# Optimization experiments

Hardware: AMD Instinct MI355X
Metric: run time of the kernel (lower is better)

The kernel has to match this reference:

```python
import jax, jax.numpy as jnp
import numpy as np

EMBED_DIM = 768
NUM_HEADS = 12
HEAD_DIM = EMBED_DIM // NUM_HEADS
SCALING = HEAD_DIM ** -0.5
B, S = 2, 2048


def setup_inputs() -> dict:
    key = jax.random.key(0)
    k1, k2, k3 = jax.random.split(key, 3)
    x_q = jax.random.normal(k1, (B, S, EMBED_DIM), dtype=jnp.float32)
    # xavier-uniform-ish scaling for weights
    lim_qkv = (6.0 / (EMBED_DIM + 3 * EMBED_DIM)) ** 0.5
    lim_out = (6.0 / (2 * EMBED_DIM)) ** 0.5
    w_qkv = jax.random.uniform(k2, (3 * EMBED_DIM, EMBED_DIM), jnp.float32, -lim_qkv, lim_qkv)
    b_qkv = jnp.zeros((3 * EMBED_DIM,), jnp.float32)
    w_out = jax.random.uniform(k3, (EMBED_DIM, EMBED_DIM), jnp.float32, -lim_out, lim_out)
    b_out = jnp.zeros((EMBED_DIM,), jnp.float32)
    return {"x_q": x_q, "w_qkv": w_qkv, "b_qkv": b_qkv, "w_out": w_out, "b_out": b_out}


def reference(x_q, w_qkv, b_qkv, w_out, b_out):
    b_sz, s_len, _ = x_q.shape
    # qkv projection: (B,S,3E) -> (B,S,3,H,hd) -> split
    qkv = x_q @ w_qkv.T + b_qkv
    qkv = qkv.reshape(b_sz, s_len, 3, NUM_HEADS, HEAD_DIM)
    q = qkv[:, :, 0].transpose(0, 2, 1, 3) * SCALING  # (B,H,S,hd)
    k = qkv[:, :, 1].transpose(0, 2, 1, 3)
    v = qkv[:, :, 2].transpose(0, 2, 1, 3)
    attn = jnp.einsum("bhsd,bhtd->bhst", q, k)  # (B,H,S,S)
    attn = jax.nn.softmax(attn.astype(jnp.float32), axis=-1).astype(attn.dtype)
    out = jnp.einsum("bhst,bhtd->bhsd", attn, v)  # (B,H,S,hd)
    out = out.transpose(0, 2, 1, 3).reshape(b_sz, s_len, EMBED_DIM)
    return out @ w_out.T + b_out
```

## Files before the change

kernel.cpp:

```cpp
#include <hip/hip_runtime.h>
#include <hip/hip_bf16.h>
#include <math.h>

typedef unsigned short u16;
typedef unsigned int u32;
typedef __attribute__((ext_vector_type(8))) short bf16x8;
typedef __attribute__((ext_vector_type(4))) short bf16x4;
typedef __attribute__((ext_vector_type(4))) float f32x4;

#define EMBED 768
#define NHEADS 12
#define HDIM 64
#define NBATCH 2
#define SEQ 2048
#define NTOK 4096
#define QKV_N 2304
#define BHTOT 24
#define QSCALE 0.18033688011112042f

__device__ __forceinline__ u16 f2b(float f) {
    __hip_bfloat16 h = __float2bfloat16(f);
    return __builtin_bit_cast(u16, h);
}
__device__ __forceinline__ u32 pk2(float a, float b) {
    return (u32)f2b(a) | ((u32)f2b(b) << 16);
}
__device__ __forceinline__ f32x4 mfma32(bf16x8 a, bf16x8 b, f32x4 c) {
    return __builtin_amdgcn_mfma_f32_16x16x32_bf16(a, b, c, 0, 0, 0);
}
#if __has_builtin(__builtin_amdgcn_mfma_f32_16x16x16_bf16)
__device__ __forceinline__ f32x4 mfma16(bf16x4 a, bf16x4 b, f32x4 c) {
    return __builtin_amdgcn_mfma_f32_16x16x16_bf16(a, b, c, 0, 0, 0);
}
#else
__device__ __forceinline__ f32x4 mfma16(bf16x4 a, bf16x4 b, f32x4 c) {
    return __builtin_amdgcn_mfma_f32_16x16x16bf16_1k(a, b, c, 0, 0, 0);
}
#endif

__device__ __forceinline__ float exp2_hw(float x) {
#if __has_builtin(__builtin_amdgcn_exp2f)
    return __builtin_amdgcn_exp2f(x);
#else
    float r;
    asm("v_exp_f32 %0, %1" : "=v"(r) : "v"(x));
    return r;
#endif
}

__device__ __forceinline__ void async16(const u16* g, u16* l) {
    __builtin_amdgcn_global_load_lds(
        (const __attribute__((address_space(1))) unsigned int*)g,
        (__attribute__((address_space(3))) unsigned int*)l,
        16, 0, 0);
}

__global__ __launch_bounds__(256)
void cast_kernel(const float* __restrict__ s0, u16* __restrict__ d0, int n0,
                 const float* __restrict__ s1, u16* __restrict__ d1, int n1,
                 const float* __restrict__ s2, u16* __restrict__ d2, int n2)
{
    int idx = (blockIdx.x * 256 + threadIdx.x) * 4;
    const float* s; u16* d; int i;
    if (idx < n0)            { s = s0; d = d0; i = idx; }
    else if (idx < n0 + n1)  { s = s1; d = d1; i = idx - n0; }
    else                     { s = s2; d = d2; i = idx - n0 - n1; if (i >= n2) return; }
    float4 v = *(const float4*)&s[i];
    ushort4 o;
    o.x = f2b(v.x); o.y = f2b(v.y); o.z = f2b(v.z); o.w = f2b(v.w);
    *(ushort4*)&d[i] = o;
}

__global__ __launch_bounds__(256)
void qkv_gemm(const u16* __restrict__ A, const u16* __restrict__ W,
              const float* __restrict__ bias,
              u16* __restrict__ Qb, u16* __restrict__ Kb, u16* __restrict__ VT)
{
    __shared__ __align__(16) u16 smem[4 * 8192];
    u16* As = smem;
    u16* Bs = smem + 2 * 8192;
    const int m0 = blockIdx.x * 128;
    const int n0 = blockIdx.y * 128;
    const int tid = threadIdx.x;
    const int w = tid >> 6, l = tid & 63;
    const int c = l & 15, q = l >> 4;
    const int wm = (w >> 1) * 64, wn = (w & 1) * 64;
    const int r8 = l >> 3, ch = l & 7;
    const int gch = ch ^ r8;

    #pragma unroll
    for (int j = 0; j < 4; ++j) {
        int row = w * 32 + j * 8 + r8;
        int seg = (w * 32 + j * 8) * 64;
        async16(&A[(size_t)(m0 + row) * EMBED + gch * 8], &As[seg + l * 8]);
        async16(&W[(size_t)(n0 + row) * EMBED + gch * 8], &Bs[seg + l * 8]);
    }

    f32x4 acc[4][4] = {};
    const int NK = EMBED / 64;

    #pragma unroll 2
    for (int kt = 0; kt < NK; ++kt) {
        const int cur = kt & 1;
        __syncthreads();
        if (kt + 1 < NK) {
            int k0 = (kt + 1) * 64;
            #pragma unroll
            for (int j = 0; j < 4; ++j) {
                int row = w * 32 + j * 8 + r8;
                int seg = (cur ^ 1) * 8192 + (w * 32 + j * 8) * 64;
                async16(&A[(size_t)(m0 + row) * EMBED + k0 + gch * 8], &As[seg + l * 8]);
                async16(&W[(size_t)(n0 + row) * EMBED + k0 + gch * 8], &Bs[seg + l * 8]);
            }
        }
        const u16* Ab = As + cur * 8192;
        const u16* Bb = Bs + cur * 8192;
        #pragma unroll
        for (int ks = 0; ks < 2; ++ks) {
            const int cs = (((ks << 2) | q) ^ (c & 7)) << 3;
            bf16x8 af[4], bfr[4];
            #pragma unroll
            for (int i = 0; i < 4; ++i)
                af[i] = *(const bf16x8*)&Ab[(wm + i * 16 + c) * 64 + cs];
            #pragma unroll
            for (int j = 0; j < 4; ++j)
                bfr[j] = *(const bf16x8*)&Bb[(wn + j * 16 + c) * 64 + cs];
            #pragma unroll
            for (int i = 0; i < 4; ++i)
                #pragma unroll
                for (int j = 0; j < 4; ++j)
                    acc[i][j] = mfma32(af[i], bfr[j], acc[i][j]);
        }
    }

    const int p = n0 / EMBED;
    const int ncol0 = n0 + wn;
    const int h = (ncol0 % EMBED) / HDIM;
    const int mrow0 = m0 + wm;
    const int b = mrow0 >> 11;
    const int s0 = mrow0 & (SEQ - 1);

    if (p < 2) {
        u16* dst = (p == 0) ? Qb : Kb;
        const float mul = (p == 0) ? QSCALE : 1.0f;
        #pragma unroll
        for (int j = 0; j < 4; ++j) {
            int n = ncol0 + j * 16 + c;
            int d = j * 16 + c;
            float bval = bias[n];
            #pragma unroll
            for (int i = 0; i < 4; ++i) {
                #pragma unroll
                for (int r = 0; r < 4; ++r) {
                    int s = s0 + i * 16 + q * 4 + r;
                    float v = (acc[i][j][r] + bval) * mul;
                    dst[(((size_t)(b * NHEADS + h)) * SEQ + s) * HDIM + d] = f2b(v);
                }
            }
        }
    } else {
        __syncthreads();
        u16* T = smem + w * (64 * 72);
        #pragma unroll
        for (int j = 0; j < 4; ++j) {
            int n = ncol0 + j * 16 + c;
            float bval = bias[n];
            #pragma unroll
            for (int i = 0; i < 4; ++i) {
                uint2 pr;
                pr.x = pk2(acc[i][j][0] + bval, acc[i][j][1] + bval);
                pr.y = pk2(acc[i][j][2] + bval, acc[i][j][3] + bval);
                *(uint2*)&T[(j * 16 + c) * 72 + i * 16 + q * 4] = pr;
            }
        }
        const size_t vtbase = ((size_t)(b * NHEADS + h)) * HDIM * SEQ + s0;
        #pragma unroll
        for (int ii = 0; ii < 8; ++ii) {
            int d = (l >> 3) + 8 * ii;
            int sch = (l & 7) * 8;
            uint4 vv = *(const uint4*)&T[d * 72 + sch];
            *(uint4*)&VT[vtbase + (size_t)d * SEQ + sch] = vv;
        }
    }
}

__global__ __launch_bounds__(256, 3)
void attn_kernel(const u16* __restrict__ Qb, const u16* __restrict__ Kb,
                 const u16* __restrict__ VT, u16* __restrict__ AO)
{
    __shared__ __align__(16) u16 Ks[3][4096];
    __shared__ __align__(16) u16 Vs[3][4096];

    const int blk = blockIdx.x;
    const int g = blk & 7, kk = blk >> 3;
    const int bh = g * 3 + (kk >> 5);
    const int qt = kk & 31;

    const int tid = threadIdx.x;
    const int w = tid >> 6, l = tid & 63;
    const int c = l & 15, q = l >> 4;

    const u16* qg = Qb + ((size_t)bh * SEQ + qt * 64 + w * 16) * HDIM;
    const u16* kg = Kb + ((size_t)bh * SEQ) * HDIM;
    const u16* vg = VT + ((size_t)bh * HDIM) * SEQ;

    const int r8 = l >> 3, ch = l & 7;
    const int gch = ch ^ r8;

    bf16x8 bq0 = *(const bf16x8*)&qg[c * HDIM + q * 8];
    bf16x8 bq1 = *(const bf16x8*)&qg[c * HDIM + 32 + q * 8];

    f32x4 o[4] = {};
    float lrow = 0.f;

    const int NT = SEQ / 64;

#define STAGE(JT, BS) {                                                       \
    int row0 = w * 16 + r8;                                                   \
    async16(&kg[(size_t)((JT) * 64 + row0) * HDIM + gch * 8],                 \
            &Ks[BS][(w * 16) * 64 + l * 8]);                                  \
    async16(&vg[(size_t)row0 * SEQ + (JT) * 64 + gch * 8],                    \
            &Vs[BS][(w * 16) * 64 + l * 8]);                                  \
    async16(&kg[(size_t)((JT) * 64 + row0 + 8) * HDIM + gch * 8],             \
            &Ks[BS][(w * 16 + 8) * 64 + l * 8]);                              \
    async16(&vg[(size_t)(row0 + 8) * SEQ + (JT) * 64 + gch * 8],              \
            &Vs[BS][(w * 16 + 8) * 64 + l * 8]);                              \
}

#define QKT(SN, BN) {                                                         \
    __builtin_amdgcn_s_setprio(1);                                            \
    _Pragma("unroll")                                                         \
    for (int kb = 0; kb < 4; ++kb) {                                          \
        bf16x8 ak0 = *(const bf16x8*)&Ks[BN][(kb * 16 + c) * 64 +             \
                                             (((q    ) ^ (c & 7)) << 3)];     \
        bf16x8 ak1 = *(const bf16x8*)&Ks[BN][(kb * 16 + c) * 64 +             \
                                             (((q | 4) ^ (c & 7)) << 3)];     \
        f32x4 zz = {};                                                        \
        zz = mfma32(ak0, bq0, zz);                                            \
        SN[kb] = mfma32(ak1, bq1, zz);                                        \
    }                                                                         \
    __builtin_amdgcn_s_setprio(0);                                            \
}

#define SOFTPV(SC, BC) {                                                      \
    _Pragma("unroll")                                                         \
    for (int kb = 0; kb < 4; ++kb) {                                          \
        float p0 = exp2_hw(SC[kb][0]);                                        \
        float p1 = exp2_hw(SC[kb][1]);                                        \
        float p2 = exp2_hw(SC[kb][2]);                                        \
        float p3 = exp2_hw(SC[kb][3]);                                        \
        SC[kb][0] = p0; SC[kb][1] = p1; SC[kb][2] = p2; SC[kb][3] = p3;       \
        lrow += (p0 + p1) + (p2 + p3);                                        \
    }                                                                         \
    bf16x4 bp[4];                                                             \
    _Pragma("unroll")                                                         \
    for (int kb = 0; kb < 4; ++kb) {                                          \
        uint2 pr;                                                             \
        pr.x = pk2(SC[kb][0], SC[kb][1]);                                     \
        pr.y = pk2(SC[kb][2], SC[kb][3]);                                     \
        bp[kb] = __builtin_bit_cast(bf16x4, pr);                              \
    }                                                                         \
    __builtin_amdgcn_s_setprio(1);                                            \
    _Pragma("unroll")                                                         \
    for (int db = 0; db < 4; ++db) {                                          \
        bf16x4 av[4];                                                         \
        _Pragma("unroll")                                                     \
        for (int kb = 0; kb < 4; ++kb)                                        \
            av[kb] = *(const bf16x4*)&Vs[BC][(db * 16 + c) * 64 +             \
                      (((2 * kb + (q >> 1)) ^ (c & 7)) << 3) + ((q & 1) << 2)]; \
        f32x4 t = o[db];                                                      \
        _Pragma("unroll")                                                     \
        for (int kb = 0; kb < 4; ++kb) t = mfma16(av[kb], bp[kb], t);         \
        o[db] = t;                                                            \
    }                                                                         \
    __builtin_amdgcn_s_setprio(0);                                            \
}

#define BODY(J, SC, SN, BC, BN, BS) {                                         \
    asm volatile("s_waitcnt vmcnt(0)" ::: "memory");                          \
    __builtin_amdgcn_s_barrier();                                             \
    if ((J) + 2 < NT) STAGE((J) + 2, BS);                                     \
    if ((J) + 1 < NT) QKT(SN, BN);                                            \
    SOFTPV(SC, BC);                                                           \
}

    f32x4 scA[4], scB[4];

    STAGE(0, 0);
    STAGE(1, 1);
    asm volatile("s_waitcnt vmcnt(4)" ::: "memory");
    __builtin_amdgcn_s_barrier();
    QKT(scA, 0);

    for (int jb = 0; jb < 30; jb += 6) {
        BODY(jb + 0, scA, scB, 0, 1, 2);
        BODY(jb + 1, scB, scA, 1, 2, 0);
        BODY(jb + 2, scA, scB, 2, 0, 1);
        BODY(jb + 3, scB, scA, 0, 1, 2);
        BODY(jb + 4, scA, scB, 1, 2, 0);
        BODY(jb + 5, scB, scA, 2, 0, 1);
    }
    BODY(30, scA, scB, 0, 1, 2);
    SOFTPV(scB, 1);

#undef STAGE
#undef QKT
#undef SOFTPV
#undef BODY

    lrow += __shfl_xor(lrow, 16);
    lrow += __shfl_xor(lrow, 32);
    float inv = 1.0f / lrow;

    const int b = bh / NHEADS, h = bh % NHEADS;
    const int s = qt * 64 + w * 16 + c;
    u16* ao = AO + ((size_t)(b * SEQ + s)) * EMBED + h * HDIM;
    #pragma unroll
    for (int db = 0; db < 4; ++db) {
        uint2 oo;
        oo.x = pk2(o[db][0] * inv, o[db][1] * inv);
        oo.y = pk2(o[db][2] * inv, o[db][3] * inv);
        *(uint2*)&ao[db * 16 + q * 4] = oo;
    }
}

__global__ __launch_bounds__(256)
void out_gemm(const u16* __restrict__ A, const u16* __restrict__ W,
              const float* __restrict__ bias, float* __restrict__ out)
{
    __shared__ __align__(16) u16 As[2][8192];
    __shared__ __align__(16) u16 Bs[2][4096];
    const int m0 = blockIdx.x * 128;
    const int n0 = blockIdx.y * 64;
    const int tid = threadIdx.x;
    const int w = tid >> 6, l = tid & 63;
    const int c = l & 15, q = l >> 4;
    const int wm = w * 32;
    const int r8 = l >> 3, ch = l & 7;
    const int gch = ch ^ r8;

    #pragma unroll
    for (int j = 0; j < 4; ++j) {
        int row = w * 32 + j * 8 + r8;
        async16(&A[(size_t)(m0 + row) * EMBED + gch * 8],
                &As[0][(w * 32 + j * 8) * 64 + l * 8]);
    }
    #pragma unroll
    for (int j = 0; j < 2; ++j) {
        int row = w * 16 + j * 8 + r8;
        async16(&W[(size_t)(n0 + row) * EMBED + gch * 8],
                &Bs[0][(w * 16 + j * 8) * 64 + l * 8]);
    }

    f32x4 acc[2][4] = {};
    const int NK = EMBED / 64;

    #pragma unroll 2
    for (int kt = 0; kt < NK; ++kt) {
        const int cur = kt & 1;
        __syncthreads();
        if (kt + 1 < NK) {
            int k0 = (kt + 1) * 64;
            #pragma unroll
            for (int j = 0; j < 4; ++j) {
                int row = w * 32 + j * 8 + r8;
                async16(&A[(size_t)(m0 + row) * EMBED + k0 + gch * 8],
                        &As[cur ^ 1][(w * 32 + j * 8) * 64 + l * 8]);
            }
            #pragma unroll
            for (int j = 0; j < 2; ++j) {
                int row = w * 16 + j * 8 + r8;
                async16(&W[(size_t)(n0 + row) * EMBED + k0 + gch * 8],
                        &Bs[cur ^ 1][(w * 16 + j * 8) * 64 + l * 8]);
            }
        }
        #pragma unroll
        for (int ks = 0; ks < 2; ++ks) {
            const int cs = (((ks << 2) | q) ^ (c & 7)) << 3;
            bf16x8 af[2], bfr[4];
            #pragma unroll
            for (int i = 0; i < 2; ++i)
                af[i] = *(const bf16x8*)&As[cur][(wm + i * 16 + c) * 64 + cs];
            #pragma unroll
            for (int j = 0; j < 4; ++j)
                bfr[j] = *(const bf16x8*)&Bs[cur][(j * 16 + c) * 64 + cs];
            #pragma unroll
            for (int i = 0; i < 2; ++i)
                #pragma unroll
                for (int j = 0; j < 4; ++j)
                    acc[i][j] = mfma32(af[i], bfr[j], acc[i][j]);
        }
    }

    #pragma unroll
    for (int j = 0; j < 4; ++j) {
        int n = n0 + j * 16 + c;
        float bval = bias[n];
        #pragma unroll
        for (int i = 0; i < 2; ++i) {
            #pragma unroll
            for (int r = 0; r < 4; ++r) {
                int m = m0 + wm + i * 16 + q * 4 + r;
                out[(size_t)m * EMBED + n] = acc[i][j][r] + bval;
            }
        }
    }
}

extern "C" void kernel_launch(void* const* d_in, const int* in_sizes, int n_in,
                              void* d_out, int out_size, void* d_ws, size_t ws_size,
                              hipStream_t stream)
{
    const float* x    = (const float*)d_in[0];
    const float* wqkv = (const float*)d_in[1];
    const float* bqkv = (const float*)d_in[2];
    const float* wout = (const float*)d_in[3];
    const float* bout = (const float*)d_in[4];
    float* out = (float*)d_out;

    const int nx  = NTOK * EMBED;
    const int nwq = QKV_N * EMBED;
    const int nwo = EMBED * EMBED;
    const size_t per = (size_t)NBATCH * NHEADS * SEQ * HDIM;

    u16* xb    = (u16*)d_ws;
    u16* wqkvb = xb + nx;
    u16* woutb = wqkvb + nwq;
    u16* Qb    = woutb + nwo;
    u16* Kb    = Qb + per;
    u16* VT    = Kb + per;
    u16* AO    = VT + per;

    int castTot = (nx + nwq + nwo) / 4;
    cast_kernel<<<castTot / 256, 256, 0, stream>>>(x, xb, nx, wqkv, wqkvb, nwq, wout, woutb, nwo);

    dim3 g1(NTOK / 128, QKV_N / 128);
    qkv_gemm<<<g1, 256, 0, stream>>>(xb, wqkvb, bqkv, Qb, Kb, VT);

    attn_kernel<<<BHTOT * 32, 256, 0, stream>>>(Qb, Kb, VT, AO);

    dim3 g3(NTOK / 128, EMBED / 64);
    out_gemm<<<g3, 256, 0, stream>>>(AO, woutb, bout, out);
}
```

Baseline: 155.2 us.

## Split attention KV tile across waves instead of query rows, reduce via LDS

Each wave now handles all 64 query rows of the block against its own 16-key slice of each KV tile, instead of 16 query rows against all 64 keys. K and V fragment loads from LDS drop to one per wave per step, while Q fragments held in registers grow fourfold and the accumulators grow to 4x4 tiles. A cross-wave reduction of the partial outputs and row sums through LDS scratch, with several barriers, is added at the end. The intent is to cut LDS read traffic in the inner loop, at the cost of more register pressure under the launch bound of 3 blocks and a longer epilogue.

```diff
diff --git a/kernel.cpp b/kernel.cpp
--- a/kernel.cpp
+++ b/kernel.cpp
@@ -200,18 +200,22 @@
     const int w = tid >> 6, l = tid & 63;
     const int c = l & 15, q = l >> 4;
 
-    const u16* qg = Qb + ((size_t)bh * SEQ + qt * 64 + w * 16) * HDIM;
+    const u16* qg = Qb + ((size_t)bh * SEQ + qt * 64) * HDIM;
     const u16* kg = Kb + ((size_t)bh * SEQ) * HDIM;
     const u16* vg = VT + ((size_t)bh * HDIM) * SEQ;
 
     const int r8 = l >> 3, ch = l & 7;
     const int gch = ch ^ r8;
 
-    bf16x8 bq0 = *(const bf16x8*)&qg[c * HDIM + q * 8];
-    bf16x8 bq1 = *(const bf16x8*)&qg[c * HDIM + 32 + q * 8];
-
-    f32x4 o[4] = {};
-    float lrow = 0.f;
+    bf16x8 bq[4][2];
+    #pragma unroll
+    for (int qb = 0; qb < 4; ++qb) {
+        bq[qb][0] = *(const bf16x8*)&qg[(qb * 16 + c) * HDIM + q * 8];
+        bq[qb][1] = *(const bf16x8*)&qg[(qb * 16 + c) * HDIM + 32 + q * 8];
+    }
+
+    f32x4 o[4][4] = {};
+    float lrow[4] = {0.f, 0.f, 0.f, 0.f};
 
     const int NT = SEQ / 64;
 
@@ -229,49 +233,45 @@
 
 #define QKT(SN, BN) {                                                         \
     __builtin_amdgcn_s_setprio(1);                                            \
+    bf16x8 ak0 = *(const bf16x8*)&Ks[BN][(w * 16 + c) * 64 +                  \
+                                         (((q    ) ^ (c & 7)) << 3)];         \
+    bf16x8 ak1 = *(const bf16x8*)&Ks[BN][(w * 16 + c) * 64 +                  \
+                                         (((q | 4) ^ (c & 7)) << 3)];         \
     _Pragma("unroll")                                                         \
-    for (int kb = 0; kb < 4; ++kb) {                                          \
-        bf16x8 ak0 = *(const bf16x8*)&Ks[BN][(kb * 16 + c) * 64 +             \
-                                             (((q    ) ^ (c & 7)) << 3)];     \
-        bf16x8 ak1 = *(const bf16x8*)&Ks[BN][(kb * 16 + c) * 64 +             \
-                                             (((q | 4) ^ (c & 7)) << 3)];     \
+    for (int qb = 0; qb < 4; ++qb) {                                          \
         f32x4 zz = {};                                                        \
-        zz = mfma32(ak0, bq0, zz);                                            \
-        SN[kb] = mfma32(ak1, bq1, zz);                                        \
+        zz = mfma32(ak0, bq[qb][0], zz);                                      \
+        SN[qb] = mfma32(ak1, bq[qb][1], zz);                                  \
     }                                                                         \
     __builtin_amdgcn_s_setprio(0);                                            \
 }
 
 #define SOFTPV(SC, BC) {                                                      \
     _Pragma("unroll")                                                         \
-    for (int kb = 0; kb < 4; ++kb) {                                          \
-        float p0 = exp2_hw(SC[kb][0]);                                        \
-        float p1 = exp2_hw(SC[kb][1]);                                        \
-        float p2 = exp2_hw(SC[kb][2]);                                        \
-        float p3 = exp2_hw(SC[kb][3]);                                        \
-        SC[kb][0] = p0; SC[kb][1] = p1; SC[kb][2] = p2; SC[kb][3] = p3;       \
-        lrow += (p0 + p1) + (p2 + p3);                                        \
+    for (int qb = 0; qb < 4; ++qb) {                                          \
+        float p0 = exp2_hw(SC[qb][0]);                                        \
+        float p1 = exp2_hw(SC[qb][1]);                                        \
+        float p2 = exp2_hw(SC[qb][2]);                                        \
+        float p3 = exp2_hw(SC[qb][3]);                                        \
+        SC[qb][0] = p0; SC[qb][1] = p1; SC[qb][2] = p2; SC[qb][3] = p3;       \
+        lrow[qb] += (p0 + p1) + (p2 + p3);                                    \
     }                                                                         \
     bf16x4 bp[4];                                                             \
     _Pragma("unroll")                                                         \
-    for (int kb = 0; kb < 4; ++kb) {                                          \
+    for (int qb = 0; qb < 4; ++qb) {                                          \
         uint2 pr;                                                             \
-        pr.x = pk2(SC[kb][0], SC[kb][1]);                                     \
-        pr.y = pk2(SC[kb][2], SC[kb][3]);                                     \
-        bp[kb] = __builtin_bit_cast(bf16x4, pr);                              \
+        pr.x = pk2(SC[qb][0], SC[qb][1]);                                     \
+        pr.y = pk2(SC[qb][2], SC[qb][3]);                                     \
+        bp[qb] = __builtin_bit_cast(bf16x4, pr);                              \
     }                                                                         \
     __builtin_amdgcn_s_setprio(1);                                            \
     _Pragma("unroll")                                                         \
     for (int db = 0; db < 4; ++db) {                                          \
-        bf16x4 av[4];                                                         \
+        bf16x4 av = *(const bf16x4*)&Vs[BC][(db * 16 + c) * 64 +              \
+                  (((2 * w + (q >> 1)) ^ (c & 7)) << 3) + ((q & 1) << 2)];    \
         _Pragma("unroll")                                                     \
-        for (int kb = 0; kb < 4; ++kb)                                        \
-            av[kb] = *(const bf16x4*)&Vs[BC][(db * 16 + c) * 64 +             \
-                      (((2 * kb + (q >> 1)) ^ (c & 7)) << 3) + ((q & 1) << 2)]; \
-        f32x4 t = o[db];                                                      \
-        _Pragma("unroll")                                                     \
-        for (int kb = 0; kb < 4; ++kb) t = mfma16(av[kb], bp[kb], t);         \
-        o[db] = t;                                                            \
+        for (int qb = 0; qb < 4; ++qb)                                        \
+            o[db][qb] = mfma16(av, bp[qb], o[db][qb]);                        \
     }                                                                         \
     __builtin_amdgcn_s_setprio(0);                                            \
 }
@@ -308,9 +308,38 @@
 #undef SOFTPV
 #undef BODY
 
-    lrow += __shfl_xor(lrow, 16);
-    lrow += __shfl_xor(lrow, 32);
-    float inv = 1.0f / lrow;
+    __syncthreads();
+    float* SCR = (float*)&Ks[0][0];
+    float* LR  = (float*)&Vs[0][0];
+
+    #pragma unroll
+    for (int qb = 0; qb < 4; ++qb) {
+        lrow[qb] += __shfl_xor(lrow[qb], 16);
+        lrow[qb] += __shfl_xor(lrow[qb], 32);
+    }
+    if (q == 0) {
+        #pragma unroll
+        for (int qb = 0; qb < 4; ++qb)
+            LR[(w * 4 + qb) * 16 + c] = lrow[qb];
+    }
+
+    #pragma unroll
+    for (int db = 0; db < 4; ++db) {
+        __syncthreads();
+        #pragma unroll
+        for (int qb = 0; qb < 4; ++qb)
+            *(f32x4*)&SCR[(w * 4 + qb) * 320 + c * 20 + q * 4] = o[db][qb];
+        __syncthreads();
+        f32x4 s0 = *(const f32x4*)&SCR[(0 * 4 + w) * 320 + c * 20 + q * 4];
+        f32x4 s1 = *(const f32x4*)&SCR[(1 * 4 + w) * 320 + c * 20 + q * 4];
+        f32x4 s2 = *(const f32x4*)&SCR[(2 * 4 + w) * 320 + c * 20 + q * 4];
+        f32x4 s3 = *(const f32x4*)&SCR[(3 * 4 + w) * 320 + c * 20 + q * 4];
+        o[db][0] = (s0 + s1) + (s2 + s3);
+    }
+
+    float lsum = (LR[(0 * 4 + w) * 16 + c] + LR[(1 * 4 + w) * 16 + c]) +
+                 (LR[(2 * 4 + w) * 16 + c] + LR[(3 * 4 + w) * 16 + c]);
+    float inv = 1.0f / lsum;
 
     const int b = bh / NHEADS, h = bh % NHEADS;
     const int s = qt * 64 + w * 16 + c;
@@ -318,8 +347,8 @@
     #pragma unroll
     for (int db = 0; db < 4; ++db) {
         uint2 oo;
-        oo.x = pk2(o[db][0] * inv, o[db][1] * inv);
-        oo.y = pk2(o[db][2] * inv, o[db][3] * inv);
+        oo.x = pk2(o[db][0][0] * inv, o[db][0][1] * inv);
+        oo.y = pk2(o[db][0][2] * inv, o[db][0][3] * inv);
         *(uint2*)&ao[db * 16 + q * 4] = oo;
     }
 }
```

New measurement: 312.9 us. 2.02x slower.

## Split attention warps 2x2 over query and key halves with LDS reduction

Applied to the files above, without the earlier changes.

Each wave now handles 32 query rows against half of each 64-key tile, instead of 16 query rows against the full tile. Each K and V fragment read from LDS therefore feeds two query blocks, roughly halving per-wave LDS read traffic per MFMA. The two key-half partial outputs and row sums are combined through shared memory (reusing the K buffer) before normalization and store. In exchange, each wave holds more accumulator registers and the epilogue gains an extra LDS round trip with two barriers.

```diff
diff --git a/kernel.cpp b/kernel.cpp
--- a/kernel.cpp
+++ b/kernel.cpp
@@ -199,19 +199,24 @@
     const int tid = threadIdx.x;
     const int w = tid >> 6, l = tid & 63;
     const int c = l & 15, q = l >> 4;
-
-    const u16* qg = Qb + ((size_t)bh * SEQ + qt * 64 + w * 16) * HDIM;
+    const int wq = w >> 1, wk = w & 1;
+
+    const u16* qg = Qb + ((size_t)bh * SEQ + qt * 64 + wq * 32) * HDIM;
     const u16* kg = Kb + ((size_t)bh * SEQ) * HDIM;
     const u16* vg = VT + ((size_t)bh * HDIM) * SEQ;
 
     const int r8 = l >> 3, ch = l & 7;
     const int gch = ch ^ r8;
 
-    bf16x8 bq0 = *(const bf16x8*)&qg[c * HDIM + q * 8];
-    bf16x8 bq1 = *(const bf16x8*)&qg[c * HDIM + 32 + q * 8];
-
-    f32x4 o[4] = {};
-    float lrow = 0.f;
+    bf16x8 bq[2][2];
+    #pragma unroll
+    for (int qb2 = 0; qb2 < 2; ++qb2) {
+        bq[qb2][0] = *(const bf16x8*)&qg[(qb2 * 16 + c) * HDIM + q * 8];
+        bq[qb2][1] = *(const bf16x8*)&qg[(qb2 * 16 + c) * HDIM + 32 + q * 8];
+    }
+
+    f32x4 o[4][2] = {};
+    float lrow[2] = {0.f, 0.f};
 
     const int NT = SEQ / 64;
 
@@ -230,48 +235,56 @@
 #define QKT(SN, BN) {                                                         \
     __builtin_amdgcn_s_setprio(1);                                            \
     _Pragma("unroll")                                                         \
-    for (int kb = 0; kb < 4; ++kb) {                                          \
-        bf16x8 ak0 = *(const bf16x8*)&Ks[BN][(kb * 16 + c) * 64 +             \
+    for (int kb2 = 0; kb2 < 2; ++kb2) {                                       \
+        bf16x8 ak0 = *(const bf16x8*)&Ks[BN][(wk * 32 + kb2 * 16 + c) * 64 +  \
                                              (((q    ) ^ (c & 7)) << 3)];     \
-        bf16x8 ak1 = *(const bf16x8*)&Ks[BN][(kb * 16 + c) * 64 +             \
+        bf16x8 ak1 = *(const bf16x8*)&Ks[BN][(wk * 32 + kb2 * 16 + c) * 64 +  \
                                              (((q | 4) ^ (c & 7)) << 3)];     \
-        f32x4 zz = {};                                                        \
-        zz = mfma32(ak0, bq0, zz);                                            \
-        SN[kb] = mfma32(ak1, bq1, zz);                                        \
+        _Pragma("unroll")                                                     \
+        for (int qb2 = 0; qb2 < 2; ++qb2) {                                   \
+            f32x4 zz = {};                                                    \
+            zz = mfma32(ak0, bq[qb2][0], zz);                                 \
+            SN[kb2][qb2] = mfma32(ak1, bq[qb2][1], zz);                       \
+        }                                                                     \
     }                                                                         \
     __builtin_amdgcn_s_setprio(0);                                            \
 }
 
 #define SOFTPV(SC, BC) {                                                      \
     _Pragma("unroll")                                                         \
-    for (int kb = 0; kb < 4; ++kb) {                                          \
-        float p0 = exp2_hw(SC[kb][0]);                                        \
-        float p1 = exp2_hw(SC[kb][1]);                                        \
-        float p2 = exp2_hw(SC[kb][2]);                                        \
-        float p3 = exp2_hw(SC[kb][3]);                                        \
-        SC[kb][0] = p0; SC[kb][1] = p1; SC[kb][2] = p2; SC[kb][3] = p3;       \
-        lrow += (p0 + p1) + (p2 + p3);                                        \
-    }                                                                         \
-    bf16x4 bp[4];                                                             \
+    for (int kb2 = 0; kb2 < 2; ++kb2)                                         \
+        _Pragma("unroll")                                                     \
+        for (int qb2 = 0; qb2 < 2; ++qb2) {                                   \
+            float p0 = exp2_hw(SC[kb2][qb2][0]);                              \
+            float p1 = exp2_hw(SC[kb2][qb2][1]);                              \
+            float p2 = exp2_hw(SC[kb2][qb2][2]);                              \
+            float p3 = exp2_hw(SC[kb2][qb2][3]);                              \
+            SC[kb2][qb2][0] = p0; SC[kb2][qb2][1] = p1;                       \
+            SC[kb2][qb2][2] = p2; SC[kb2][qb2][3] = p3;                       \
+            lrow[qb2] += (p0 + p1) + (p2 + p3);                               \
+        }                                                                     \
+    bf16x4 bp[2][2];                                                          \
     _Pragma("unroll")                                                         \
-    for (int kb = 0; kb < 4; ++kb) {                                          \
-        uint2 pr;                                                             \
-        pr.x = pk2(SC[kb][0], SC[kb][1]);                                     \
-        pr.y = pk2(SC[kb][2], SC[kb][3]);                                     \
-        bp[kb] = __builtin_bit_cast(bf16x4, pr);                              \
-    }                                                                         \
+    for (int kb2 = 0; kb2 < 2; ++kb2)                                         \
+        _Pragma("unroll")                                                     \
+        for (int qb2 = 0; qb2 < 2; ++qb2) {                                   \
+            uint2 pr;                                                         \
+            pr.x = pk2(SC[kb2][qb2][0], SC[kb2][qb2][1]);                     \
+            pr.y = pk2(SC[kb2][qb2][2], SC[kb2][qb2][3]);                     \
+            bp[kb2][qb2] = __builtin_bit_cast(bf16x4, pr);                    \
+        }                                                                     \
     __builtin_amdgcn_s_setprio(1);                                            \
     _Pragma("unroll")                                                         \
     for (int db = 0; db < 4; ++db) {                                          \
-        bf16x4 av[4];                                                         \
+        bf16x4 av0 = *(const bf16x4*)&Vs[BC][(db * 16 + c) * 64 +             \
+                  (((4 * wk     + (q >> 1)) ^ (c & 7)) << 3) + ((q & 1) << 2)]; \
+        bf16x4 av1 = *(const bf16x4*)&Vs[BC][(db * 16 + c) * 64 +             \
+                  (((4 * wk + 2 + (q >> 1)) ^ (c & 7)) << 3) + ((q & 1) << 2)]; \
         _Pragma("unroll")                                                     \
-        for (int kb = 0; kb < 4; ++kb)                                        \
-            av[kb] = *(const bf16x4*)&Vs[BC][(db * 16 + c) * 64 +             \
-                      (((2 * kb + (q >> 1)) ^ (c & 7)) << 3) + ((q & 1) << 2)]; \
-        f32x4 t = o[db];                                                      \
-        _Pragma("unroll")                                                     \
-        for (int kb = 0; kb < 4; ++kb) t = mfma16(av[kb], bp[kb], t);         \
-        o[db] = t;                                                            \
+        for (int qb2 = 0; qb2 < 2; ++qb2) {                                   \
+            o[db][qb2] = mfma16(av0, bp[0][qb2], o[db][qb2]);                 \
+            o[db][qb2] = mfma16(av1, bp[1][qb2], o[db][qb2]);                 \
+        }                                                                     \
     }                                                                         \
     __builtin_amdgcn_s_setprio(0);                                            \
 }
@@ -284,7 +297,7 @@
     SOFTPV(SC, BC);                                                           \
 }
 
-    f32x4 scA[4], scB[4];
+    f32x4 scA[2][2], scB[2][2];
 
     STAGE(0, 0);
     STAGE(1, 1);
@@ -308,19 +321,49 @@
 #undef SOFTPV
 #undef BODY
 
-    lrow += __shfl_xor(lrow, 16);
-    lrow += __shfl_xor(lrow, 32);
-    float inv = 1.0f / lrow;
-
-    const int b = bh / NHEADS, h = bh % NHEADS;
-    const int s = qt * 64 + w * 16 + c;
-    u16* ao = AO + ((size_t)(b * SEQ + s)) * EMBED + h * HDIM;
-    #pragma unroll
-    for (int db = 0; db < 4; ++db) {
-        uint2 oo;
-        oo.x = pk2(o[db][0] * inv, o[db][1] * inv);
-        oo.y = pk2(o[db][2] * inv, o[db][3] * inv);
-        *(uint2*)&ao[db * 16 + q * 4] = oo;
+    #pragma unroll
+    for (int qb2 = 0; qb2 < 2; ++qb2) {
+        lrow[qb2] += __shfl_xor(lrow[qb2], 16);
+        lrow[qb2] += __shfl_xor(lrow[qb2], 32);
+    }
+
+    __syncthreads();
+    float* SCR = (float*)&Ks[0][0];
+    float* LR  = SCR + 4096;
+
+    if (wk == 1) {
+        #pragma unroll
+        for (int db = 0; db < 4; ++db)
+            #pragma unroll
+            for (int qb2 = 0; qb2 < 2; ++qb2)
+                *(f32x4*)&SCR[((wq * 8 + db * 2 + qb2) << 8) + l * 4] = o[db][qb2];
+        if (q == 0) {
+            LR[(wq * 2 + 0) * 16 + c] = lrow[0];
+            LR[(wq * 2 + 1) * 16 + c] = lrow[1];
+        }
+    }
+    __syncthreads();
+
+    if (wk == 0) {
+        float inv[2];
+        #pragma unroll
+        for (int qb2 = 0; qb2 < 2; ++qb2)
+            inv[qb2] = 1.0f / (lrow[qb2] + LR[(wq * 2 + qb2) * 16 + c]);
+        const int b = bh / NHEADS, h = bh % NHEADS;
+        #pragma unroll
+        for (int qb2 = 0; qb2 < 2; ++qb2) {
+            const int s = qt * 64 + wq * 32 + qb2 * 16 + c;
+            u16* ao = AO + ((size_t)(b * SEQ + s)) * EMBED + h * HDIM;
+            #pragma unroll
+            for (int db = 0; db < 4; ++db) {
+                f32x4 part = *(const f32x4*)&SCR[((wq * 8 + db * 2 + qb2) << 8) + l * 4];
+                f32x4 t = o[db][qb2] + part;
+                uint2 oo;
+                oo.x = pk2(t[0] * inv[qb2], t[1] * inv[qb2]);
+                oo.y = pk2(t[2] * inv[qb2], t[3] * inv[qb2]);
+                *(uint2*)&ao[db * 16 + q * 4] = oo;
+            }
+        }
     }
 }
 
```

Measured after the change: 149.9 us. 3.5% less time.
